# Kernel optimization log

Measured on AMD Instinct MI355X. Metric: run time of the kernel, lower is better.

## Reference

```python
import jax, jax.numpy as jnp
import numpy as np

B, L, INPUT_DIM = 2, 2048, 512
D_MODEL, N_HEAD, MLP_HIDDEN = 1024, 16, 4096
CONTEXT_LENGTH = 2048
EPS = 1e-5


def _layer_norm(x, w, b):
    mu = jnp.mean(x, axis=-1, keepdims=True)
    var = jnp.mean(jnp.square(x - mu), axis=-1, keepdims=True)
    return (x - mu) * jax.lax.rsqrt(var + EPS) * w + b


def setup_inputs() -> dict:
    key = jax.random.key(0)
    ks = jax.random.split(key, 12)
    s = 0.02
    return {
        "x": jax.random.normal(ks[0], (B, L, INPUT_DIM), dtype=jnp.float32),
        "wte_w": jax.random.normal(ks[1], (INPUT_DIM, D_MODEL), dtype=jnp.float32) * s,
        "wte_b": jnp.zeros((D_MODEL,), dtype=jnp.float32),
        "wpe": jax.random.normal(ks[2], (CONTEXT_LENGTH, D_MODEL), dtype=jnp.float32) * s,
        "ln1_w": jnp.ones((D_MODEL,), dtype=jnp.float32),
        "ln1_b": jnp.zeros((D_MODEL,), dtype=jnp.float32),
        "kq_w": jax.random.normal(ks[3], (D_MODEL, 2 * D_MODEL), dtype=jnp.float32) * s,
        "kq_b": jnp.zeros((2 * D_MODEL,), dtype=jnp.float32),
        "v_w": jax.random.normal(ks[4], (D_MODEL, D_MODEL), dtype=jnp.float32) * s,
        "v_b": jnp.zeros((D_MODEL,), dtype=jnp.float32),
        "ao_w": jax.random.normal(ks[5], (D_MODEL, D_MODEL), dtype=jnp.float32) * s,
        "ao_b": jnp.zeros((D_MODEL,), dtype=jnp.float32),
        "ln2_w": jnp.ones((D_MODEL,), dtype=jnp.float32),
        "ln2_b": jnp.zeros((D_MODEL,), dtype=jnp.float32),
        "fc_w": jax.random.normal(ks[6], (D_MODEL, MLP_HIDDEN), dtype=jnp.float32) * s,
        "fc_b": jnp.zeros((MLP_HIDDEN,), dtype=jnp.float32),
        "proj_w": jax.random.normal(ks[7], (MLP_HIDDEN, INPUT_DIM), dtype=jnp.float32) * s,
        "proj_b": jnp.zeros((INPUT_DIM,), dtype=jnp.float32),
    }


def reference(x, wte_w, wte_b, wpe, ln1_w, ln1_b, kq_w, kq_b, v_w, v_b,
              ao_w, ao_b, ln2_w, ln2_b, fc_w, fc_b, proj_w, proj_b):
    b, l, _ = x.shape
    hd = D_MODEL // N_HEAD
    # token "embedding" (linear) + learnable positional embedding
    h = x @ wte_w + wte_b + wpe[:l]                      # [B, L, D]
    hn = _layer_norm(h, ln1_w, ln1_b)                    # ln_1
    # attention (kq fused linear -> split gives k first, then q)
    kq = hn @ kq_w + kq_b                                # [B, L, 2D]
    k, q = kq[..., :D_MODEL], kq[..., D_MODEL:]
    v = hn @ v_w + v_b
    q = q.reshape(b, l, N_HEAD, hd).transpose(0, 2, 1, 3)  # [B, H, L, hd]
    k = k.reshape(b, l, N_HEAD, hd).transpose(0, 2, 1, 3)
    v = v.reshape(b, l, N_HEAD, hd).transpose(0, 2, 1, 3)
    scale = 1.0 / jnp.sqrt(jnp.asarray(hd, dtype=q.dtype))
    scores = jnp.einsum('bhqd,bhkd->bhqk', q, k) * scale  # [B, H, L, L]
    causal = jnp.tril(jnp.ones((l, l), dtype=bool))
    scores = jnp.where(causal, scores, jnp.asarray(-jnp.inf, dtype=scores.dtype))
    attn = jax.nn.softmax(scores, axis=-1)
    o = jnp.einsum('bhqk,bhkd->bhqd', attn, v)            # [B, H, L, hd]
    o = o.transpose(0, 2, 1, 3).reshape(b, l, D_MODEL)
    o = o @ ao_w + ao_b
    attn_out = hn + o                                     # residual recorded by Block
    xo = _layer_norm(attn_out, ln2_w, ln2_b)              # ln_2
    # MLP head to input_dim (exact GELU, matching torch nn.GELU default)
    out = jax.nn.gelu(xo @ fc_w + fc_b, approximate=False) @ proj_w + proj_b
    return (out, attn_out)
```

## Files before the change

kernel.cpp:

```cpp
#include <hip/hip_runtime.h>
#include <hip/hip_bf16.h>
#include <cmath>

#define D_MODEL   1024
#define N_HEAD    16
#define HEAD_DIM  64
#define SEQ_LEN   2048
#define NBATCH    2
#define M_TOTAL   (NBATCH * SEQ_LEN)
#define IN_DIM    512
#define MLP_HID   4096

typedef __attribute__((ext_vector_type(8))) short short8;
typedef __attribute__((ext_vector_type(4))) short short4v;
typedef __attribute__((ext_vector_type(4))) float floatx4;

typedef const __attribute__((address_space(1))) void* gas_ptr;
typedef __attribute__((address_space(3))) void* las_ptr;

__device__ __forceinline__ void async_copy16(const void* g, void* l) {
  __builtin_amdgcn_global_load_lds((gas_ptr)g, (las_ptr)l, 16, 0, 0);
}


__global__ __launch_bounds__(256) void k_prep(const float* __restrict__ wte_w,
                                              const float* __restrict__ kq_w,
                                              const float* __restrict__ v_w,
                                              const float* __restrict__ ao_w,
                                              const float* __restrict__ fc_w,
                                              const float* __restrict__ proj_w,
                                              const float* __restrict__ x,
                                              __hip_bfloat16* __restrict__ wT,
                                              __hip_bfloat16* __restrict__ x_bf) {
  const int bid = blockIdx.x;
  const float* in; __hip_bfloat16* out; int K, N, local;
  if (bid < 128)        { in = wte_w;  out = wT;           K = IN_DIM;  N = D_MODEL;     local = bid;        }
  else if (bid < 640)   { in = kq_w;   out = wT +  524288; K = D_MODEL; N = 2 * D_MODEL; local = bid - 128;  }
  else if (bid < 896)   { in = v_w;    out = wT + 2621440; K = D_MODEL; N = D_MODEL;     local = bid - 640;  }
  else if (bid < 1152)  { in = ao_w;   out = wT + 3670016; K = D_MODEL; N = D_MODEL;     local = bid - 896;  }
  else if (bid < 2176)  { in = fc_w;   out = wT + 4718592; K = D_MODEL; N = MLP_HID;     local = bid - 1152; }
  else if (bid < 2688)  { in = proj_w; out = wT + 8912896; K = MLP_HID; N = IN_DIM;      local = bid - 2176; }
  else {
    int i = (bid - 2688) * 256 + threadIdx.x;
    float4 v = ((const float4*)x)[i];
    short4v o;
    ((__hip_bfloat16*)&o)[0] = __float2bfloat16(v.x);
    ((__hip_bfloat16*)&o)[1] = __float2bfloat16(v.y);
    ((__hip_bfloat16*)&o)[2] = __float2bfloat16(v.z);
    ((__hip_bfloat16*)&o)[3] = __float2bfloat16(v.w);
    ((short4v*)x_bf)[i] = o;
    return;
  }
  __shared__ __hip_bfloat16 t[64][73];
  const int ntx = N >> 6;
  const int n0 = (local % ntx) * 64, k0 = (local / ntx) * 64;
  const int tx = threadIdx.x & 7, ty = threadIdx.x >> 3;
#pragma unroll
  for (int i = 0; i < 64; i += 32) {
    const float* src = in + (size_t)(k0 + ty + i) * N + n0 + tx * 8;
    float4 v0 = ((const float4*)src)[0];
    float4 v1 = ((const float4*)src)[1];
    t[ty + i][tx * 8 + 0] = __float2bfloat16(v0.x);
    t[ty + i][tx * 8 + 1] = __float2bfloat16(v0.y);
    t[ty + i][tx * 8 + 2] = __float2bfloat16(v0.z);
    t[ty + i][tx * 8 + 3] = __float2bfloat16(v0.w);
    t[ty + i][tx * 8 + 4] = __float2bfloat16(v1.x);
    t[ty + i][tx * 8 + 5] = __float2bfloat16(v1.y);
    t[ty + i][tx * 8 + 6] = __float2bfloat16(v1.z);
    t[ty + i][tx * 8 + 7] = __float2bfloat16(v1.w);
  }
  __syncthreads();
#pragma unroll
  for (int i = 0; i < 64; i += 32) {
    int nr = ty + i;
    short8 o;
#pragma unroll
    for (int j = 0; j < 8; j++) ((__hip_bfloat16*)&o)[j] = t[tx * 8 + j][nr];
    *(short8*)(out + (size_t)(n0 + nr) * K + k0 + tx * 8) = o;
  }
}

__global__ __launch_bounds__(256) void k_reduce_proj(const __hip_bfloat16* __restrict__ part,
                                                     const float* __restrict__ bias,
                                                     float* __restrict__ out) {
  int i = blockIdx.x * 256 + threadIdx.x;
  const size_t SP8 = (size_t)M_TOTAL * IN_DIM / 8;
  int cb = (i & (IN_DIM / 8 - 1)) * 2;
  float4 s0 = ((const float4*)bias)[cb];
  float4 s1 = ((const float4*)bias)[cb + 1];
#pragma unroll
  for (int j = 0; j < 8; j++) {
    short8 v = ((const short8*)part)[i + j * SP8];
    s0.x += __bfloat162float(((const __hip_bfloat16*)&v)[0]);
    s0.y += __bfloat162float(((const __hip_bfloat16*)&v)[1]);
    s0.z += __bfloat162float(((const __hip_bfloat16*)&v)[2]);
    s0.w += __bfloat162float(((const __hip_bfloat16*)&v)[3]);
    s1.x += __bfloat162float(((const __hip_bfloat16*)&v)[4]);
    s1.y += __bfloat162float(((const __hip_bfloat16*)&v)[5]);
    s1.z += __bfloat162float(((const __hip_bfloat16*)&v)[6]);
    s1.w += __bfloat162float(((const __hip_bfloat16*)&v)[7]);
  }
  ((float4*)out)[i * 2]     = s0;
  ((float4*)out)[i * 2 + 1] = s1;
}


__global__ __launch_bounds__(256) void k_ln1_combine(const float* __restrict__ part,
                                                     const float* __restrict__ wb,
                                                     const float* __restrict__ wpe,
                                                     const float* __restrict__ lw,
                                                     const float* __restrict__ lb,
                                                     __hip_bfloat16* __restrict__ out_bf) {
  int row = blockIdx.x;
  int l = row & (SEQ_LEN - 1);
  float4 a = ((const float4*)(part + (size_t)row * D_MODEL))[threadIdx.x];
  float4 c = ((const float4*)(part + (size_t)(M_TOTAL + row) * D_MODEL))[threadIdx.x];
  float4 wb4 = ((const float4*)wb)[threadIdx.x];
  float4 pe4 = ((const float4*)(wpe + (size_t)l * D_MODEL))[threadIdx.x];
  float4 v;
  v.x = a.x + c.x + wb4.x + pe4.x;
  v.y = a.y + c.y + wb4.y + pe4.y;
  v.z = a.z + c.z + wb4.z + pe4.z;
  v.w = a.w + c.w + wb4.w + pe4.w;
  float s  = v.x + v.y + v.z + v.w;
  float sq = v.x * v.x + v.y * v.y + v.z * v.z + v.w * v.w;
#pragma unroll
  for (int o = 1; o < 64; o <<= 1) { s += __shfl_xor(s, o); sq += __shfl_xor(sq, o); }
  __shared__ float ss[4], ssq[4];
  int lane = threadIdx.x & 63, wv = threadIdx.x >> 6;
  if (lane == 0) { ss[wv] = s; ssq[wv] = sq; }
  __syncthreads();
  s  = ss[0] + ss[1] + ss[2] + ss[3];
  sq = ssq[0] + ssq[1] + ssq[2] + ssq[3];
  float mu  = s * (1.f / D_MODEL);
  float var = sq * (1.f / D_MODEL) - mu * mu;
  float rs  = rsqrtf(var + 1e-5f);
  float4 lw4 = ((const float4*)lw)[threadIdx.x];
  float4 lb4 = ((const float4*)lb)[threadIdx.x];
  size_t base = (size_t)row * D_MODEL + threadIdx.x * 4;
  out_bf[base + 0] = __float2bfloat16((v.x - mu) * rs * lw4.x + lb4.x);
  out_bf[base + 1] = __float2bfloat16((v.y - mu) * rs * lw4.y + lb4.y);
  out_bf[base + 2] = __float2bfloat16((v.z - mu) * rs * lw4.z + lb4.z);
  out_bf[base + 3] = __float2bfloat16((v.w - mu) * rs * lw4.w + lb4.w);
}

__global__ __launch_bounds__(256) void k_ln2_combine(const float* __restrict__ part,
                                                     const float* __restrict__ bias,
                                                     const __hip_bfloat16* __restrict__ hn,
                                                     const float* __restrict__ lw,
                                                     const float* __restrict__ lb,
                                                     float* __restrict__ attn_out,
                                                     __hip_bfloat16* __restrict__ out_bf) {
  int row = blockIdx.x;
  float4 a = ((const float4*)(part + (size_t)row * D_MODEL))[threadIdx.x];
  float4 c = ((const float4*)(part + (size_t)(M_TOTAL + row) * D_MODEL))[threadIdx.x];
  float4 b4 = ((const float4*)bias)[threadIdx.x];
  short4v h4 = ((const short4v*)(hn + (size_t)row * D_MODEL))[threadIdx.x];
  float4 v;
  v.x = a.x + c.x + b4.x + __bfloat162float(((const __hip_bfloat16*)&h4)[0]);
  v.y = a.y + c.y + b4.y + __bfloat162float(((const __hip_bfloat16*)&h4)[1]);
  v.z = a.z + c.z + b4.z + __bfloat162float(((const __hip_bfloat16*)&h4)[2]);
  v.w = a.w + c.w + b4.w + __bfloat162float(((const __hip_bfloat16*)&h4)[3]);
  ((float4*)(attn_out + (size_t)row * D_MODEL))[threadIdx.x] = v;
  float s  = v.x + v.y + v.z + v.w;
  float sq = v.x * v.x + v.y * v.y + v.z * v.z + v.w * v.w;
#pragma unroll
  for (int o = 1; o < 64; o <<= 1) { s += __shfl_xor(s, o); sq += __shfl_xor(sq, o); }
  __shared__ float ss[4], ssq[4];
  int lane = threadIdx.x & 63, wv = threadIdx.x >> 6;
  if (lane == 0) { ss[wv] = s; ssq[wv] = sq; }
  __syncthreads();
  s  = ss[0] + ss[1] + ss[2] + ss[3];
  sq = ssq[0] + ssq[1] + ssq[2] + ssq[3];
  float mu  = s * (1.f / D_MODEL);
  float var = sq * (1.f / D_MODEL) - mu * mu;
  float rs  = rsqrtf(var + 1e-5f);
  float4 lw4 = ((const float4*)lw)[threadIdx.x];
  float4 lb4 = ((const float4*)lb)[threadIdx.x];
  size_t base = (size_t)row * D_MODEL + threadIdx.x * 4;
  out_bf[base + 0] = __float2bfloat16((v.x - mu) * rs * lw4.x + lb4.x);
  out_bf[base + 1] = __float2bfloat16((v.y - mu) * rs * lw4.y + lb4.y);
  out_bf[base + 2] = __float2bfloat16((v.z - mu) * rs * lw4.z + lb4.z);
  out_bf[base + 3] = __float2bfloat16((v.w - mu) * rs * lw4.w + lb4.w);
}


struct KQVEpi {
  const float* kq_b; const float* v_b;
  __hip_bfloat16* kb; __hip_bfloat16* qb; __hip_bfloat16* vt;
  __device__ void operator()(int row, int col, const floatx4& v) const {
    int b = row >> 11, l = row & (SEQ_LEN - 1);
    int which = col >> 10, c = col & (D_MODEL - 1);
    int head = c >> 6, d = c & 63;
    if (which == 2) {
      float bias = v_b[c];
      short4v o;
#pragma unroll
      for (int t = 0; t < 4; t++)
        ((__hip_bfloat16*)&o)[t] = __float2bfloat16(v[t] + bias);
      *(short4v*)(vt + ((size_t)(b * N_HEAD + head) * HEAD_DIM + d) * SEQ_LEN + l) = o;
    } else {
      float bias = kq_b[col];
      float scale = (which == 1) ? 0.125f : 1.f;
      __hip_bfloat16* dst = (which == 0) ? kb : qb;
#pragma unroll
      for (int t = 0; t < 4; t++)
        dst[((size_t)(b * N_HEAD + head) * SEQ_LEN + l + t) * HEAD_DIM + d] =
            __float2bfloat16((v[t] + bias) * scale);
    }
  }
};

struct FCEpi {
  const float* bias; __hip_bfloat16* act;
  __device__ void operator()(int row, int col, const floatx4& v) const {
    float bi = bias[col];
#pragma unroll
    for (int t = 0; t < 4; t++) {
      float x = v[t] + bi;
      float g = 0.5f * x * (1.f + erff(x * 0.70710678118654752f));
      act[(size_t)(row + t) * MLP_HID + col] = __float2bfloat16(g);
    }
  }
};

struct PartEpi {
  float* part;
  __device__ void operator()(int row, int col, const floatx4& v) const {
    float* p = part + (size_t)blockIdx.z * ((size_t)M_TOTAL * D_MODEL) +
               (size_t)row * D_MODEL + col;
#pragma unroll
    for (int t = 0; t < 4; t++) p[(size_t)t * D_MODEL] = v[t];
  }
};

struct PartBf16Epi {
  __hip_bfloat16* part;
  __device__ void operator()(int row, int col, const floatx4& v) const {
    __hip_bfloat16* p = part + (size_t)blockIdx.z * ((size_t)M_TOTAL * IN_DIM) +
                        (size_t)row * IN_DIM + col;
#pragma unroll
    for (int t = 0; t < 4; t++) p[(size_t)t * IN_DIM] = __float2bfloat16(v[t]);
  }
};


template <class Epi>
__global__ __launch_bounds__(256) void k_gemm(const __hip_bfloat16* __restrict__ A,
                                              const __hip_bfloat16* __restrict__ Bt,
                                              int M, int N, int K, int Kchunk, Epi epi) {
  __shared__ __align__(16) short As[128 * 64];
  __shared__ __align__(16) short Bs[128 * 64];
  const int tid  = threadIdx.x;
  const int lane = tid & 63;
  const int w    = tid >> 6;
  const int wm   = (w >> 1) << 6;
  const int wn   = (w & 1) << 6;
  const int r    = lane & 15;
  const int quad = lane >> 4;
  const int m0 = blockIdx.y << 7;
  const int n0 = blockIdx.x << 7;
  const int koff = blockIdx.z * Kchunk;

  const __hip_bfloat16* pa[4];
  const __hip_bfloat16* pb[4];
#pragma unroll
  for (int j = 0; j < 4; j++) {
    int s = tid + j * 256;
    int row = s >> 3;
    int c = (s & 7) ^ (row & 7);
    pa[j] = A  + (size_t)(m0 + row) * K + (c << 3) + koff;
    pb[j] = Bt + (size_t)(n0 + row) * K + (c << 3) + koff;
  }

  floatx4 acc[4][4];
#pragma unroll
  for (int i = 0; i < 4; i++)
#pragma unroll
    for (int j = 0; j < 4; j++) acc[i][j] = (floatx4){0.f, 0.f, 0.f, 0.f};

  int aoff[2][4], boff[2][4];
#pragma unroll
  for (int kk = 0; kk < 2; kk++)
#pragma unroll
    for (int i = 0; i < 4; i++) {
      int pc = ((quad + (kk << 2)) ^ (r & 7)) << 3;
      aoff[kk][i] = (wm + i * 16 + r) * 64 + pc;
      boff[kk][i] = (wn + i * 16 + r) * 64 + pc;
    }

  for (int k0 = 0; k0 < Kchunk; k0 += 64) {
    __syncthreads();
#pragma unroll
    for (int j = 0; j < 4; j++) {
      async_copy16(pa[j] + k0, &As[(tid + j * 256) * 8]);
      async_copy16(pb[j] + k0, &Bs[(tid + j * 256) * 8]);
    }
    __syncthreads();
#pragma unroll
    for (int kk = 0; kk < 2; kk++) {
      short8 fa[4], fb[4];
#pragma unroll
      for (int i = 0; i < 4; i++) {
        fa[i] = *(const short8*)&As[aoff[kk][i]];
        fb[i] = *(const short8*)&Bs[boff[kk][i]];
      }
#pragma unroll
      for (int i = 0; i < 4; i++)
#pragma unroll
        for (int j = 0; j < 4; j++)
          acc[i][j] = __builtin_amdgcn_mfma_f32_16x16x32_bf16(fa[i], fb[j], acc[i][j], 0, 0, 0);
    }
  }

#pragma unroll
  for (int i = 0; i < 4; i++)
#pragma unroll
    for (int j = 0; j < 4; j++)
      epi(m0 + wm + i * 16 + quad * 4, n0 + wn + j * 16 + r, acc[i][j]);
}

template <class Epi>
static void launch_gemm(const __hip_bfloat16* A, const __hip_bfloat16* Bt,
                        int M, int N, int K, Epi epi, hipStream_t s) {
  dim3 grid(N / 128, M / 128, 1);
  k_gemm<Epi><<<grid, 256, 0, s>>>(A, Bt, M, N, K, K, epi);
}


#define STAGE_A(BUF, H, KT)                                                       \
  do {                                                                            \
    async_copy16(ga + (size_t)((H) * 128) * K + (KT) * 64,                        \
                 &As[BUF][(tid + (H) * 1024) * 8]);                               \
    async_copy16(ga + (size_t)((H) * 128 + 64) * K + (KT) * 64,                   \
                 &As[BUF][(tid + (H) * 1024 + 512) * 8]);                         \
  } while (0)

#define STAGE_B(BUF, H, KT)                                                       \
  do {                                                                            \
    async_copy16(gb + (size_t)((H) * 128) * K + (KT) * 64,                        \
                 &Bs[BUF][(tid + (H) * 1024) * 8]);                               \
    async_copy16(gb + (size_t)((H) * 128 + 64) * K + (KT) * 64,                   \
                 &Bs[BUF][(tid + (H) * 1024 + 512) * 8]);                         \
  } while (0)

#define MFMA_BLK(IO, JO, BFX)                                                     \
  _Pragma("unroll") for (int i = 0; i < 4; i++) {                                 \
    _Pragma("unroll") for (int j = 0; j < 2; j++) {                               \
      acc[(IO) + i][(JO) + j] = __builtin_amdgcn_mfma_f32_16x16x32_bf16(          \
          af[i][0], BFX[j][0], acc[(IO) + i][(JO) + j], 0, 0, 0);                 \
      acc[(IO) + i][(JO) + j] = __builtin_amdgcn_mfma_f32_16x16x32_bf16(          \
          af[i][1], BFX[j][1], acc[(IO) + i][(JO) + j], 0, 0, 0);                 \
    }                                                                             \
  }

#define GTILE(T, BUF)                                                             \
  {                                                                               \
    _Pragma("unroll") for (int i = 0; i < 4; i++) {                               \
      af[i][0] = *(const short8*)&As[BUF][arb[i] + pc0];                          \
      af[i][1] = *(const short8*)&As[BUF][arb[i] + pc1];                          \
    }                                                                             \
    _Pragma("unroll") for (int j = 0; j < 2; j++) {                               \
      bf0[j][0] = *(const short8*)&Bs[BUF][brb[j] + pc0];                         \
      bf0[j][1] = *(const short8*)&Bs[BUF][brb[j] + pc1];                         \
    }                                                                             \
    if ((T) + 1 < nt) { STAGE_A((BUF) ^ 1, 1, (T) + 1); }                         \
    __builtin_amdgcn_s_barrier();                                                 \
    asm volatile("s_waitcnt lgkmcnt(0)" ::: "memory");                            \
    __builtin_amdgcn_s_setprio(1);                                                \
    MFMA_BLK(0, 0, bf0)                                                           \
    __builtin_amdgcn_s_setprio(0);                                                \
    __builtin_amdgcn_s_barrier();                                                 \
    _Pragma("unroll") for (int j = 0; j < 2; j++) {                               \
      bf1[j][0] = *(const short8*)&Bs[BUF][brb[j] + 8192 + pc0];                  \
      bf1[j][1] = *(const short8*)&Bs[BUF][brb[j] + 8192 + pc1];                  \
    }                                                                             \
    if ((T) + 2 < nt) { STAGE_A(BUF, 0, (T) + 2); }                               \
    __builtin_amdgcn_s_barrier();                                                 \
    asm volatile("s_waitcnt lgkmcnt(0)" ::: "memory");                            \
    __builtin_amdgcn_s_setprio(1);                                                \
    MFMA_BLK(0, 2, bf1)                                                           \
    __builtin_amdgcn_s_setprio(0);                                                \
    __builtin_amdgcn_s_barrier();                                                 \
    _Pragma("unroll") for (int i = 0; i < 4; i++) {                               \
      af[i][0] = *(const short8*)&As[BUF][arb[i] + 8192 + pc0];                   \
      af[i][1] = *(const short8*)&As[BUF][arb[i] + 8192 + pc1];                   \
    }                                                                             \
    if ((T) + 2 < nt) { STAGE_B(BUF, 0, (T) + 2); }                               \
    __builtin_amdgcn_s_barrier();                                                 \
    asm volatile("s_waitcnt lgkmcnt(0)" ::: "memory");                            \
    __builtin_amdgcn_s_setprio(1);                                                \
    MFMA_BLK(4, 0, bf0)                                                           \
    __builtin_amdgcn_s_setprio(0);                                                \
    __builtin_amdgcn_s_barrier();                                                 \
    if ((T) + 2 < nt) { STAGE_B(BUF, 1, (T) + 2); }                               \
    __builtin_amdgcn_s_setprio(1);                                                \
    MFMA_BLK(4, 2, bf1)                                                           \
    __builtin_amdgcn_s_setprio(0);                                                \
    if ((T) + 2 < nt) {                                                           \
      asm volatile("s_waitcnt vmcnt(6)" ::: "memory");                            \
    } else {                                                                      \
      asm volatile("s_waitcnt vmcnt(0)" ::: "memory");                            \
    }                                                                             \
    __builtin_amdgcn_s_barrier();                                                 \
  }

template <class Epi>
__global__ __launch_bounds__(512, 2) void k_gemm256(const __hip_bfloat16* __restrict__ A,
                                                    const __hip_bfloat16* __restrict__ Bt,
                                                    int M, int N, int K, int Kchunk, Epi epi) {
  (void)M; (void)N;
  __shared__ __align__(16) short As[2][16384];
  __shared__ __align__(16) short Bs[2][16384];
  const int tid  = threadIdx.x;
  const int lane = tid & 63;
  const int w    = tid >> 6;
  const int wr   = w >> 2;
  const int wc   = w & 3;
  const int r    = lane & 15;
  const int quad = lane >> 4;
  const int m0 = blockIdx.y << 8;
  const int n0 = blockIdx.x << 8;
  const int koff = blockIdx.z * Kchunk;
  const int nt = Kchunk >> 6;

  const int sr = tid >> 3;
  const int sc = (tid & 7) ^ (sr & 7);
  const __hip_bfloat16* ga = A  + (size_t)(m0 + sr) * K + sc * 8 + koff;
  const __hip_bfloat16* gb = Bt + (size_t)(n0 + sr) * K + sc * 8 + koff;

  const int pc0 = ((quad    ) ^ (r & 7)) << 3;
  const int pc1 = ((quad + 4) ^ (r & 7)) << 3;
  int arb[4], brb[2];
#pragma unroll
  for (int i = 0; i < 4; i++) arb[i] = ((2 * i + wr) * 16 + r) * 64;
#pragma unroll
  for (int j = 0; j < 2; j++) brb[j] = ((4 * j + wc) * 16 + r) * 64;

  floatx4 acc[8][4];
#pragma unroll
  for (int i = 0; i < 8; i++)
#pragma unroll
    for (int j = 0; j < 4; j++) acc[i][j] = (floatx4){0.f, 0.f, 0.f, 0.f};
  short8 af[4][2], bf0[2][2], bf1[2][2];

  STAGE_A(0, 0, 0);
  STAGE_B(0, 0, 0);
  STAGE_B(0, 1, 0);
  STAGE_A(0, 1, 0);
  if (nt > 1) {
    STAGE_A(1, 0, 1);
    STAGE_B(1, 0, 1);
    STAGE_B(1, 1, 1);
    asm volatile("s_waitcnt vmcnt(6)" ::: "memory");
  } else {
    asm volatile("s_waitcnt vmcnt(0)" ::: "memory");
  }
  __builtin_amdgcn_s_barrier();

  for (int t = 0; t < nt; t += 2) {
    GTILE(t, 0)
    GTILE(t + 1, 1)
  }

#pragma unroll
  for (int i = 0; i < 8; i++)
#pragma unroll
    for (int j = 0; j < 4; j++)
      epi(m0 + (2 * i + wr) * 16 + quad * 4, n0 + (4 * j + wc) * 16 + r, acc[i][j]);
}


#define PSTR 68

#define STAGE_KV(T, P)                                                         \
  do {                                                                         \
    async_copy16(kp + (size_t)((((T) << 6)) + srow) * HEAD_DIM + sg * 8,       \
                 &Ks[P][tid * 8]);                                             \
    async_copy16(vp + (size_t)srow * SEQ_LEN + ((T) << 6) + sg * 8,            \
                 &Vs[P][tid * 8]);                                             \
  } while (0)

#define QKSUB(KT, P)                                                           \
  {                                                                            \
    const int tss = ts + ((KT) << 4);                                          \
    short4v pk0;                                                               \
    if (tss < qend) {                                                          \
      const int krow = ((KT) << 4) + r;                                        \
      short8 a0 = *(const short8*)&Ks[P][(krow * 8 + (quad ^ sw)) * 8];        \
      short8 a1 = *(const short8*)&Ks[P][(krow * 8 + ((quad ^ sw) ^ 4)) * 8];  \
      floatx4 s0 = (floatx4){0.f, 0.f, 0.f, 0.f};                              \
      s0 = __builtin_amdgcn_mfma_f32_16x16x32_bf16(a0, qf0, s0, 0, 0, 0);      \
      s0 = __builtin_amdgcn_mfma_f32_16x16x32_bf16(a1, qf1, s0, 0, 0, 0);      \
      if (tss + 15 > qbw) {                                                    \
        int off0 = qbw + r - tss;                                              \
        _Pragma("unroll") for (int tt = 0; tt < 4; tt++) {                     \
          int kl = (quad << 2) + tt;                                           \
          if (kl > off0) s0[tt] = -INFINITY;                                   \
        }                                                                      \
      }                                                                        \
      _Pragma("unroll") for (int tt = 0; tt < 4; tt++) {                       \
        float e0 = __expf(s0[tt]); ls0 += e0;                                  \
        ((__hip_bfloat16*)&pk0)[tt] = __float2bfloat16(e0);                    \
      }                                                                        \
    } else {                                                                   \
      pk0 = (short4v){0, 0, 0, 0};                                             \
    }                                                                          \
    *(short4v*)(pw + r * PSTR + ((KT) << 4) + (quad << 2)) = pk0;              \
  }

#define PVC(C, P)                                                              \
  {                                                                            \
    short8 pb0 = *(const short8*)(pw + r * PSTR + ((C) << 5) + (quad << 3));   \
    __builtin_amdgcn_s_setprio(1);                                             \
    _Pragma("unroll") for (int fd = 0; fd < 4; fd++) {                         \
      const int vrow = (fd << 4) + r;                                          \
      short8 va = *(const short8*)&Vs[P][(vrow * 8 + ((((C) << 2) + quad) ^ sw)) * 8]; \
      of[fd] = __builtin_amdgcn_mfma_f32_16x16x32_bf16(va, pb0, of[fd], 0, 0, 0); \
    }                                                                          \
    __builtin_amdgcn_s_setprio(0);                                             \
  }

#define ATILE(T, P)                                                            \
  {                                                                            \
    const int ts = (T) << 6;                                                   \
    if (ts < qend) {                                                           \
      QKSUB(0, P)                                                              \
      QKSUB(1, P)                                                              \
      PVC(0, P)                                                                \
      QKSUB(2, P)                                                              \
      QKSUB(3, P)                                                              \
      PVC(1, P)                                                                \
    }                                                                          \
    __builtin_amdgcn_s_barrier();                                              \
    if ((T) + 2 < ktiles) {                                                    \
      STAGE_KV((T) + 2, P);                                                    \
      asm volatile("s_waitcnt vmcnt(2)" ::: "memory");                         \
    } else {                                                                   \
      asm volatile("s_waitcnt vmcnt(0)" ::: "memory");                         \
    }                                                                          \
    __builtin_amdgcn_s_barrier();                                              \
    __builtin_amdgcn_sched_barrier(0);                                         \
  }

__global__ __launch_bounds__(512, 4) void k_flash_attn(const __hip_bfloat16* __restrict__ kb,
                                                       const __hip_bfloat16* __restrict__ qb,
                                                       const __hip_bfloat16* __restrict__ vtb,
                                                       __hip_bfloat16* __restrict__ ob) {
  __shared__ __align__(16) short Ks[2][64 * 64];
  __shared__ __align__(16) short Vs[2][64 * 64];
  __shared__ __align__(16) __hip_bfloat16 Pb[8][16 * PSTR];
  const int tid  = threadIdx.x;
  const int lane = tid & 63;
  const int w    = tid >> 6;
  const int r    = lane & 15;
  const int quad = lane >> 4;
  const int sw   = r & 7;
  const int bh    = blockIdx.x & 31;
  const int strip = (SEQ_LEN / 128 - 1) - (blockIdx.x >> 5);
  const int qb0   = strip << 7;
  const int qbw   = qb0 + (w << 4);
  const int qend  = qbw + 16;
  const int b = bh >> 4, h = bh & (N_HEAD - 1);

  const __hip_bfloat16* qp = qb  + ((size_t)bh * SEQ_LEN + qbw) * HEAD_DIM;
  const __hip_bfloat16* kp = kb  + (size_t)bh * SEQ_LEN * HEAD_DIM;
  const __hip_bfloat16* vp = vtb + (size_t)bh * HEAD_DIM * SEQ_LEN;
  __hip_bfloat16* pw = &Pb[w][0];

  short8 qf0 = *(const short8*)(qp + r * HEAD_DIM + quad * 8);
  short8 qf1 = *(const short8*)(qp + r * HEAD_DIM + quad * 8 + 32);

  floatx4 of[4];
#pragma unroll
  for (int i = 0; i < 4; i++) of[i] = (floatx4){0.f, 0.f, 0.f, 0.f};
  float ls0 = 0.f;

  const int srow = tid >> 3;
  const int sg = (tid & 7) ^ (srow & 7);

  const int ktiles = (qb0 + 128) >> 6;
  STAGE_KV(0, 0);
  STAGE_KV(1, 1);
  asm volatile("s_waitcnt vmcnt(2)" ::: "memory");
  __builtin_amdgcn_s_barrier();
  __builtin_amdgcn_sched_barrier(0);

  for (int t = 0; t < ktiles; t += 2) {
    ATILE(t, 0)
    ATILE(t + 1, 1)
  }

  ls0 += __shfl_xor(ls0, 16); ls0 += __shfl_xor(ls0, 32);
  float inv0 = 1.f / ls0;

  size_t orow = ((size_t)b * SEQ_LEN + qbw + r) * D_MODEL + (size_t)h * HEAD_DIM;
#pragma unroll
  for (int fd = 0; fd < 4; fd++) {
    short4v o4;
#pragma unroll
    for (int tt = 0; tt < 4; tt++)
      ((__hip_bfloat16*)&o4)[tt] = __float2bfloat16(of[fd][tt] * inv0);
    *(short4v*)(ob + orow + fd * 16 + quad * 4) = o4;
  }
}


extern "C" void kernel_launch(void* const* d_in, const int* in_sizes, int n_in,
                              void* d_out, int out_size, void* d_ws, size_t ws_size,
                              hipStream_t stream) {
  (void)in_sizes; (void)n_in; (void)out_size; (void)ws_size;
  const float* x      = (const float*)d_in[0];
  const float* wte_w  = (const float*)d_in[1];
  const float* wte_b  = (const float*)d_in[2];
  const float* wpe    = (const float*)d_in[3];
  const float* ln1_w  = (const float*)d_in[4];
  const float* ln1_b  = (const float*)d_in[5];
  const float* kq_w   = (const float*)d_in[6];
  const float* kq_b   = (const float*)d_in[7];
  const float* v_w    = (const float*)d_in[8];
  const float* v_b    = (const float*)d_in[9];
  const float* ao_w   = (const float*)d_in[10];
  const float* ao_b   = (const float*)d_in[11];
  const float* ln2_w  = (const float*)d_in[12];
  const float* ln2_b  = (const float*)d_in[13];
  const float* fc_w   = (const float*)d_in[14];
  const float* fc_b   = (const float*)d_in[15];
  const float* proj_w = (const float*)d_in[16];
  const float* proj_b = (const float*)d_in[17];

  float* out0     = (float*)d_out;
  float* attn_out = out0 + (size_t)M_TOTAL * IN_DIM;

  char* ws = (char*)d_ws;
  __hip_bfloat16* wT    = (__hip_bfloat16*)ws;
  __hip_bfloat16* x_bf  = (__hip_bfloat16*)(ws + 22 * 1048576);
  char* R1              = ws + 26 * 1048576;
  float* embed_part     = (float*)R1;
  float* ao_part        = (float*)R1;
  __hip_bfloat16* act   = (__hip_bfloat16*)R1;
  __hip_bfloat16* k_bf  = (__hip_bfloat16*)(ws + 58 * 1048576);
  __hip_bfloat16* q_bf  = (__hip_bfloat16*)(ws + 66 * 1048576);
  __hip_bfloat16* vt_bf = (__hip_bfloat16*)(ws + 74 * 1048576);
  __hip_bfloat16* o_bf  = (__hip_bfloat16*)(ws + 82 * 1048576);
  __hip_bfloat16* hn_bf = (__hip_bfloat16*)(ws + 90 * 1048576);
  __hip_bfloat16* xo_bf = k_bf;
  __hip_bfloat16* proj_part = k_bf;

  __hip_bfloat16* wteT  = wT;
  __hip_bfloat16* kqvT  = wT +  524288;
  __hip_bfloat16* aoT   = wT + 3670016;
  __hip_bfloat16* fcT   = wT + 4718592;
  __hip_bfloat16* projT = wT + 8912896;

  k_prep<<<4736, 256, 0, stream>>>(wte_w, kq_w, v_w, ao_w, fc_w, proj_w, x, wT, x_bf);

  {
    dim3 grid(D_MODEL / 128, M_TOTAL / 128, 2);
    k_gemm<PartEpi><<<grid, 256, 0, stream>>>(x_bf, wteT, M_TOTAL, D_MODEL, IN_DIM, IN_DIM / 2,
                                              PartEpi{embed_part});
  }

  k_ln1_combine<<<M_TOTAL, 256, 0, stream>>>(embed_part, wte_b, wpe, ln1_w, ln1_b, hn_bf);

  launch_gemm(hn_bf, kqvT, M_TOTAL, 3 * D_MODEL, D_MODEL,
              KQVEpi{kq_b, v_b, k_bf, q_bf, vt_bf}, stream);

  k_flash_attn<<<(SEQ_LEN / 128) * 32, 512, 0, stream>>>(k_bf, q_bf, vt_bf, o_bf);

  {
    dim3 grid(D_MODEL / 128, M_TOTAL / 128, 2);
    k_gemm<PartEpi><<<grid, 256, 0, stream>>>(o_bf, aoT, M_TOTAL, D_MODEL, D_MODEL, D_MODEL / 2,
                                              PartEpi{ao_part});
  }

  k_ln2_combine<<<M_TOTAL, 256, 0, stream>>>(ao_part, ao_b, hn_bf, ln2_w, ln2_b, attn_out, xo_bf);

  {
    dim3 grid(MLP_HID / 256, M_TOTAL / 256, 1);
    k_gemm256<FCEpi><<<grid, 512, 0, stream>>>(xo_bf, fcT, M_TOTAL, MLP_HID, D_MODEL, D_MODEL,
                                               FCEpi{fc_b, act});
  }

  {
    dim3 grid(IN_DIM / 256, M_TOTAL / 256, 8);
    k_gemm256<PartBf16Epi><<<grid, 512, 0, stream>>>(act, projT, M_TOTAL, IN_DIM, MLP_HID,
                                                     MLP_HID / 8, PartBf16Epi{proj_part});
  }
  k_reduce_proj<<<M_TOTAL * IN_DIM / 8 / 256, 256, 0, stream>>>(proj_part, proj_b, out0);
}
```

Measured before the change: 362.9 us.

## Use 64-row attention strips with 256-thread blocks and scalar weight transpose

Flash attention now processes 64 query rows per block with 4 waves instead of 128 rows with 8 waves. Each block stages each K/V tile with two async copies per thread and does all four QK subtiles before the PV accumulation. The weight-prep kernel switches from a vectorized 64x64 bf16 transpose tile to a simple 32x32 fp32 tile with scalar loads and stores. Smaller attention blocks may balance the causal workload better, but they lose the per-wave early skip and make the prep kernel's memory accesses narrower.

Result: faster. 347.4 us (-4.3%).

```diff
diff --git a/kernel.cpp b/kernel.cpp
--- a/kernel.cpp
+++ b/kernel.cpp
@@ -34,14 +34,14 @@
                                               __hip_bfloat16* __restrict__ x_bf) {
   const int bid = blockIdx.x;
   const float* in; __hip_bfloat16* out; int K, N, local;
-  if (bid < 128)        { in = wte_w;  out = wT;           K = IN_DIM;  N = D_MODEL;     local = bid;        }
-  else if (bid < 640)   { in = kq_w;   out = wT +  524288; K = D_MODEL; N = 2 * D_MODEL; local = bid - 128;  }
-  else if (bid < 896)   { in = v_w;    out = wT + 2621440; K = D_MODEL; N = D_MODEL;     local = bid - 640;  }
-  else if (bid < 1152)  { in = ao_w;   out = wT + 3670016; K = D_MODEL; N = D_MODEL;     local = bid - 896;  }
-  else if (bid < 2176)  { in = fc_w;   out = wT + 4718592; K = D_MODEL; N = MLP_HID;     local = bid - 1152; }
-  else if (bid < 2688)  { in = proj_w; out = wT + 8912896; K = MLP_HID; N = IN_DIM;      local = bid - 2176; }
+  if (bid < 512)        { in = wte_w;  out = wT;           K = IN_DIM;  N = D_MODEL;     local = bid;        }
+  else if (bid < 2560)  { in = kq_w;   out = wT +  524288; K = D_MODEL; N = 2 * D_MODEL; local = bid - 512;  }
+  else if (bid < 3584)  { in = v_w;    out = wT + 2621440; K = D_MODEL; N = D_MODEL;     local = bid - 2560; }
+  else if (bid < 4608)  { in = ao_w;   out = wT + 3670016; K = D_MODEL; N = D_MODEL;     local = bid - 3584; }
+  else if (bid < 8704)  { in = fc_w;   out = wT + 4718592; K = D_MODEL; N = MLP_HID;     local = bid - 4608; }
+  else if (bid < 10752) { in = proj_w; out = wT + 8912896; K = MLP_HID; N = IN_DIM;      local = bid - 8704; }
   else {
-    int i = (bid - 2688) * 256 + threadIdx.x;
+    int i = (bid - 10752) * 256 + threadIdx.x;
     float4 v = ((const float4*)x)[i];
     short4v o;
     ((__hip_bfloat16*)&o)[0] = __float2bfloat16(v.x);
@@ -51,33 +51,18 @@
     ((short4v*)x_bf)[i] = o;
     return;
   }
-  __shared__ __hip_bfloat16 t[64][73];
-  const int ntx = N >> 6;
-  const int n0 = (local % ntx) * 64, k0 = (local / ntx) * 64;
-  const int tx = threadIdx.x & 7, ty = threadIdx.x >> 3;
-#pragma unroll
-  for (int i = 0; i < 64; i += 32) {
-    const float* src = in + (size_t)(k0 + ty + i) * N + n0 + tx * 8;
-    float4 v0 = ((const float4*)src)[0];
-    float4 v1 = ((const float4*)src)[1];
-    t[ty + i][tx * 8 + 0] = __float2bfloat16(v0.x);
-    t[ty + i][tx * 8 + 1] = __float2bfloat16(v0.y);
-    t[ty + i][tx * 8 + 2] = __float2bfloat16(v0.z);
-    t[ty + i][tx * 8 + 3] = __float2bfloat16(v0.w);
-    t[ty + i][tx * 8 + 4] = __float2bfloat16(v1.x);
-    t[ty + i][tx * 8 + 5] = __float2bfloat16(v1.y);
-    t[ty + i][tx * 8 + 6] = __float2bfloat16(v1.z);
-    t[ty + i][tx * 8 + 7] = __float2bfloat16(v1.w);
-  }
+  __shared__ float tile[32][33];
+  const int ntx = N >> 5;
+  const int bx = local % ntx, by = local / ntx;
+  const int n0 = bx * 32, k0 = by * 32;
+  const int tx = threadIdx.x & 31, ty = threadIdx.x >> 5;
+#pragma unroll
+  for (int i = 0; i < 32; i += 8)
+    tile[ty + i][tx] = in[(size_t)(k0 + ty + i) * N + n0 + tx];
   __syncthreads();
 #pragma unroll
-  for (int i = 0; i < 64; i += 32) {
-    int nr = ty + i;
-    short8 o;
-#pragma unroll
-    for (int j = 0; j < 8; j++) ((__hip_bfloat16*)&o)[j] = t[tx * 8 + j][nr];
-    *(short8*)(out + (size_t)(n0 + nr) * K + k0 + tx * 8) = o;
-  }
+  for (int i = 0; i < 32; i += 8)
+    out[(size_t)(n0 + ty + i) * K + k0 + tx] = __float2bfloat16(tile[tx][ty + i]);
 }
 
 __global__ __launch_bounds__(256) void k_reduce_proj(const __hip_bfloat16* __restrict__ part,
@@ -475,10 +460,14 @@
 
 #define STAGE_KV(T, P)                                                         \
   do {                                                                         \
-    async_copy16(kp + (size_t)((((T) << 6)) + srow) * HEAD_DIM + sg * 8,       \
-                 &Ks[P][tid * 8]);                                             \
-    async_copy16(vp + (size_t)srow * SEQ_LEN + ((T) << 6) + sg * 8,            \
-                 &Vs[P][tid * 8]);                                             \
+    async_copy16(kp + (size_t)((((T) << 6)) + row0) * HEAD_DIM + g0 * 8,       \
+                 &Ks[P][c0 * 8]);                                              \
+    async_copy16(kp + (size_t)((((T) << 6)) + row1) * HEAD_DIM + g1 * 8,       \
+                 &Ks[P][c1 * 8]);                                              \
+    async_copy16(vp + (size_t)row0 * SEQ_LEN + ((T) << 6) + g0 * 8,            \
+                 &Vs[P][c0 * 8]);                                              \
+    async_copy16(vp + (size_t)row1 * SEQ_LEN + ((T) << 6) + g1 * 8,            \
+                 &Vs[P][c1 * 8]);                                              \
   } while (0)
 
 #define QKSUB(KT, P)                                                           \
@@ -509,33 +498,27 @@
     *(short4v*)(pw + r * PSTR + ((KT) << 4) + (quad << 2)) = pk0;              \
   }
 
-#define PVC(C, P)                                                              \
-  {                                                                            \
-    short8 pb0 = *(const short8*)(pw + r * PSTR + ((C) << 5) + (quad << 3));   \
-    __builtin_amdgcn_s_setprio(1);                                             \
-    _Pragma("unroll") for (int fd = 0; fd < 4; fd++) {                         \
-      const int vrow = (fd << 4) + r;                                          \
-      short8 va = *(const short8*)&Vs[P][(vrow * 8 + ((((C) << 2) + quad) ^ sw)) * 8]; \
-      of[fd] = __builtin_amdgcn_mfma_f32_16x16x32_bf16(va, pb0, of[fd], 0, 0, 0); \
-    }                                                                          \
-    __builtin_amdgcn_s_setprio(0);                                             \
-  }
-
 #define ATILE(T, P)                                                            \
   {                                                                            \
     const int ts = (T) << 6;                                                   \
-    if (ts < qend) {                                                           \
-      QKSUB(0, P)                                                              \
-      QKSUB(1, P)                                                              \
-      PVC(0, P)                                                                \
-      QKSUB(2, P)                                                              \
-      QKSUB(3, P)                                                              \
-      PVC(1, P)                                                                \
+    QKSUB(0, P)                                                                \
+    QKSUB(1, P)                                                                \
+    QKSUB(2, P)                                                                \
+    QKSUB(3, P)                                                                \
+    __builtin_amdgcn_s_setprio(1);                                             \
+    _Pragma("unroll") for (int c = 0; c < 2; c++) {                            \
+      short8 pb0 = *(const short8*)(pw + r * PSTR + (c << 5) + (quad << 3));   \
+      _Pragma("unroll") for (int fd = 0; fd < 4; fd++) {                       \
+        const int vrow = (fd << 4) + r;                                        \
+        short8 va = *(const short8*)&Vs[P][(vrow * 8 + (((c << 2) + quad) ^ sw)) * 8]; \
+        of[fd] = __builtin_amdgcn_mfma_f32_16x16x32_bf16(va, pb0, of[fd], 0, 0, 0); \
+      }                                                                        \
     }                                                                          \
+    __builtin_amdgcn_s_setprio(0);                                             \
     __builtin_amdgcn_s_barrier();                                              \
     if ((T) + 2 < ktiles) {                                                    \
       STAGE_KV((T) + 2, P);                                                    \
-      asm volatile("s_waitcnt vmcnt(2)" ::: "memory");                         \
+      asm volatile("s_waitcnt vmcnt(4)" ::: "memory");                         \
     } else {                                                                   \
       asm volatile("s_waitcnt vmcnt(0)" ::: "memory");                         \
     }                                                                          \
@@ -543,13 +526,13 @@
     __builtin_amdgcn_sched_barrier(0);                                         \
   }
 
-__global__ __launch_bounds__(512, 4) void k_flash_attn(const __hip_bfloat16* __restrict__ kb,
+__global__ __launch_bounds__(256, 3) void k_flash_attn(const __hip_bfloat16* __restrict__ kb,
                                                        const __hip_bfloat16* __restrict__ qb,
                                                        const __hip_bfloat16* __restrict__ vtb,
                                                        __hip_bfloat16* __restrict__ ob) {
   __shared__ __align__(16) short Ks[2][64 * 64];
   __shared__ __align__(16) short Vs[2][64 * 64];
-  __shared__ __align__(16) __hip_bfloat16 Pb[8][16 * PSTR];
+  __shared__ __align__(16) __hip_bfloat16 Pb[4][16 * PSTR];
   const int tid  = threadIdx.x;
   const int lane = tid & 63;
   const int w    = tid >> 6;
@@ -557,8 +540,8 @@
   const int quad = lane >> 4;
   const int sw   = r & 7;
   const int bh    = blockIdx.x & 31;
-  const int strip = (SEQ_LEN / 128 - 1) - (blockIdx.x >> 5);
-  const int qb0   = strip << 7;
+  const int strip = (SEQ_LEN / 64 - 1) - (blockIdx.x >> 5);
+  const int qb0   = strip << 6;
   const int qbw   = qb0 + (w << 4);
   const int qend  = qbw + 16;
   const int b = bh >> 4, h = bh & (N_HEAD - 1);
@@ -576,19 +559,24 @@
   for (int i = 0; i < 4; i++) of[i] = (floatx4){0.f, 0.f, 0.f, 0.f};
   float ls0 = 0.f;
 
-  const int srow = tid >> 3;
-  const int sg = (tid & 7) ^ (srow & 7);
-
-  const int ktiles = (qb0 + 128) >> 6;
+  const int c0 = tid, c1 = tid + 256;
+  const int row0 = c0 >> 3, g0 = (c0 & 7) ^ (row0 & 7);
+  const int row1 = c1 >> 3, g1 = (c1 & 7) ^ (row1 & 7);
+
+  const int ktiles = strip + 1;
   STAGE_KV(0, 0);
-  STAGE_KV(1, 1);
-  asm volatile("s_waitcnt vmcnt(2)" ::: "memory");
+  if (ktiles > 1) {
+    STAGE_KV(1, 1);
+    asm volatile("s_waitcnt vmcnt(4)" ::: "memory");
+  } else {
+    asm volatile("s_waitcnt vmcnt(0)" ::: "memory");
+  }
   __builtin_amdgcn_s_barrier();
   __builtin_amdgcn_sched_barrier(0);
 
   for (int t = 0; t < ktiles; t += 2) {
     ATILE(t, 0)
-    ATILE(t + 1, 1)
+    if (t + 1 < ktiles) { ATILE(t + 1, 1) }
   }
 
   ls0 += __shfl_xor(ls0, 16); ls0 += __shfl_xor(ls0, 32);
@@ -653,7 +641,7 @@
   __hip_bfloat16* fcT   = wT + 4718592;
   __hip_bfloat16* projT = wT + 8912896;
 
-  k_prep<<<4736, 256, 0, stream>>>(wte_w, kq_w, v_w, ao_w, fc_w, proj_w, x, wT, x_bf);
+  k_prep<<<12800, 256, 0, stream>>>(wte_w, kq_w, v_w, ao_w, fc_w, proj_w, x, wT, x_bf);
 
   {
     dim3 grid(D_MODEL / 128, M_TOTAL / 128, 2);
@@ -666,7 +654,7 @@
   launch_gemm(hn_bf, kqvT, M_TOTAL, 3 * D_MODEL, D_MODEL,
               KQVEpi{kq_b, v_b, k_bf, q_bf, vt_bf}, stream);
 
-  k_flash_attn<<<(SEQ_LEN / 128) * 32, 512, 0, stream>>>(k_bf, q_bf, vt_bf, o_bf);
+  k_flash_attn<<<(SEQ_LEN / 64) * 32, 256, 0, stream>>>(k_bf, q_bf, vt_bf, o_bf);
 
   {
     dim3 grid(D_MODEL / 128, M_TOTAL / 128, 2);
```
